# Optimization experiments

Hardware: AMD Instinct MI355X
Metric: run time of the kernel (lower is better)

The kernel has to match this reference:

```python
import jax, jax.numpy as jnp
from jax import lax
import numpy as np

NF = 64      # feature channels
G = 8        # deformable groups
K = 3        # kernel size
KK = K * K
NLEVEL = 3

PARAM_SHAPES = {
    "c0a_w": (64, 3, 3, 3), "c0a_b": (64,),
    "c0r_w1": (64, 64, 3, 3), "c0r_b1": (64,), "c0r_w2": (64, 64, 3, 3), "c0r_b2": (64,),
    "c0b_w": (64, 64, 3, 3), "c0b_b": (64,),
    "d_r1w1": (64, 64, 3, 3), "d_r1b1": (64,), "d_r1w2": (64, 64, 3, 3), "d_r1b2": (64,),
    "d_r2w1": (64, 64, 3, 3), "d_r2b1": (64,), "d_r2w2": (64, 64, 3, 3), "d_r2b2": (64,),
    "d_cw": (64, 64, 3, 3), "d_cb": (64,),
    "off_c1w": (64, 128, 3, 3), "off_c1b": (64,),
    "off_rw1": (64, 64, 3, 3), "off_rb1": (64,), "off_rw2": (64, 64, 3, 3), "off_rb2": (64,),
    "off_c2w": (64, 64, 3, 3), "off_c2b": (64,),
    "mrg_c1w": (64, 128, 3, 3), "mrg_c1b": (64,),
    "mrg_rw1": (64, 64, 3, 3), "mrg_rb1": (64,), "mrg_rw2": (64, 64, 3, 3), "mrg_rb2": (64,),
    "mrg_c2w": (64, 64, 3, 3), "mrg_c2b": (64,),
    "dcn_om_w": (216, 64, 3, 3), "dcn_om_b": (216,),
    "dcn_w": (64, 64, 3, 3), "dcn_b": (64,),
}


def setup_inputs() -> dict:
    key = jax.random.key(0)
    inp = {"images": jax.random.normal(key, (2, 3, 3, 160, 160), jnp.float32)}
    for i, (name, sh) in enumerate(PARAM_SHAPES.items()):
        if len(sh) == 1:
            inp[name] = jnp.zeros(sh, jnp.float32)
        else:
            inp[name] = jax.random.normal(jax.random.fold_in(key, i + 1), sh, jnp.float32) * 0.05
    return inp


def conv(x, w, b):
    y = lax.conv_general_dilated(x, w, (1, 1), 'SAME',
                                 dimension_numbers=('NCHW', 'OIHW', 'NCHW'))
    return y + b[None, :, None, None]


def lrelu(x):  # nn.LeakyReLU default slope 0.01
    return jnp.where(x >= 0, x, 0.01 * x)


def resblock(x, w1, b1, w2, b2):
    return x + conv(jax.nn.relu(conv(x, w1, b1)), w2, b2)


def maxpool3s2(x):  # MaxPool2d(3, 2, 1)
    return lax.reduce_window(x, -jnp.inf, lax.max, (1, 1, 3, 3), (1, 1, 2, 2),
                             ((0, 0), (0, 0), (1, 1), (1, 1)))


def offnet(x, c1w, c1b, rw1, rb1, rw2, rb2, c2w, c2b):
    # Conv-LReLU, then the SAME residual block applied twice (shared), Conv-LReLU
    x = lrelu(conv(x, c1w, c1b))
    x = resblock(x, rw1, rb1, rw2, rb2)
    x = resblock(x, rw1, rb1, rw2, rb2)
    return lrelu(conv(x, c2w, c2b))


def dcn(x, feat, om_w, om_b, w, b):
    # Modulated deformable conv v2 (extra_offset_mask=True): offsets/mask from feat.
    B, C, H, W = x.shape
    Cg = C // G
    om = conv(feat, om_w, om_b)                       # [B, 3*G*KK, H, W]
    o1, o2, m = jnp.split(om, 3, axis=1)
    dy = o1.reshape(B, G, KK, H, W)
    dx = o2.reshape(B, G, KK, H, W)
    mask = jax.nn.sigmoid(m).reshape(B, G, KK, H, W)
    ky, kx = jnp.meshgrid(jnp.arange(K, dtype=x.dtype) - 1,
                          jnp.arange(K, dtype=x.dtype) - 1, indexing='ij')
    py = dy + jnp.arange(H, dtype=x.dtype)[:, None] + ky.reshape(KK)[:, None, None]
    px = dx + jnp.arange(W, dtype=x.dtype) + kx.reshape(KK)[:, None, None]
    y0 = jnp.floor(py); x0 = jnp.floor(px)
    wy = py - y0; wx = px - x0
    y0i = y0.astype(jnp.int32); x0i = x0.astype(jnp.int32)
    xg = x.reshape(B, G, Cg, H * W)

    def gather(yi, xi, wt):
        valid = (yi >= 0) & (yi < H) & (xi >= 0) & (xi < W)
        idx = jnp.clip(yi, 0, H - 1) * W + jnp.clip(xi, 0, W - 1)      # [B,G,KK,H,W]
        g = jnp.take_along_axis(
            xg, jnp.broadcast_to(idx.reshape(B, G, 1, KK * H * W), (B, G, Cg, KK * H * W)),
            axis=3).reshape(B, G, Cg, KK, H, W)
        return g * (wt * valid)[:, :, None]

    val = (gather(y0i, x0i, (1 - wy) * (1 - wx))
           + gather(y0i, x0i + 1, (1 - wy) * wx)
           + gather(y0i + 1, x0i, wy * (1 - wx))
           + gather(y0i + 1, x0i + 1, wy * wx))
    val = val * mask[:, :, None]                      # [B,G,Cg,KK,H,W]
    wr = w.reshape(w.shape[0], G, Cg, KK)
    return jnp.einsum('bgckhw,ogck->bohw', val, wr) + b[None, :, None, None]


def reference(images, c0a_w, c0a_b, c0r_w1, c0r_b1, c0r_w2, c0r_b2, c0b_w, c0b_b,
              d_r1w1, d_r1b1, d_r1w2, d_r1b2, d_r2w1, d_r2b1, d_r2w2, d_r2b2, d_cw, d_cb,
              off_c1w, off_c1b, off_rw1, off_rb1, off_rw2, off_rb2, off_c2w, off_c2b,
              mrg_c1w, mrg_c1b, mrg_rw1, mrg_rb1, mrg_rw2, mrg_rb2, mrg_c2w, mrg_c2b,
              dcn_om_w, dcn_om_b, dcn_w, dcn_b):
    b, n, c, h, w = images.shape
    x = images.reshape(b * n, c, h, w)
    x = conv(x, c0a_w, c0a_b)
    x = resblock(x, c0r_w1, c0r_b1, c0r_w2, c0r_b2)
    feat = lrelu(conv(x, c0b_w, c0b_b))
    pyrs = [feat]
    for _ in range(NLEVEL - 1):  # downs share one parameter set ([module]*n)
        y = resblock(pyrs[-1], d_r1w1, d_r1b1, d_r1w2, d_r1b2)
        y = resblock(y, d_r2w1, d_r2b1, d_r2w2, d_r2b2)
        y = lrelu(maxpool3s2(conv(y, d_cw, d_cb)))
        pyrs.append(y)
    laps = [p.reshape(b, n, NF, p.shape[-2], p.shape[-1]) for p in pyrs]
    offp = (off_c1w, off_c1b, off_rw1, off_rb1, off_rw2, off_rb2, off_c2w, off_c2b)
    mrgp = (mrg_c1w, mrg_c1b, mrg_rw1, mrg_rb1, mrg_rw2, mrg_rb2, mrg_c2w, mrg_c2b)
    cv = n // 2
    for view in range(n):  # sequential in-place update (center view mutates mid-loop)
        po = offnet(jnp.concatenate([laps[-1][:, cv], laps[-1][:, view]], 1), *offp)
        laps[-1] = laps[-1].at[:, view].set(
            dcn(laps[-1][:, view], po, dcn_om_w, dcn_om_b, dcn_w, dcn_b))
        for level in range(NLEVEL - 2, -1, -1):
            cf = laps[level][:, cv]
            lf = laps[level][:, view]
            off = offnet(jnp.concatenate([cf, lf], 1), *offp)
            B_, C_, H_, W_ = po.shape
            po_up = jax.image.resize(po, (B_, C_, H_ * 2, W_ * 2), 'bilinear')
            off = offnet(jnp.concatenate([off, po_up * 2.0], 1), *mrgp)
            laps[level] = laps[level].at[:, view].set(
                dcn(lf, off, dcn_om_w, dcn_om_b, dcn_w, dcn_b))
            po = off
    return tuple(laps)
```

## Files before the change

### kernel.cpp

```cpp
#include <hip/hip_runtime.h>
#include <math.h>

using short8 = __attribute__((ext_vector_type(8))) short;
using f32x4  = __attribute__((ext_vector_type(4))) float;

struct Tab8 { long o[8]; };

__device__ __forceinline__ unsigned short f2bf(float f) {
    unsigned u = __builtin_bit_cast(unsigned, f);
    unsigned r = u + 0x7FFFu + ((u >> 16) & 1u);
    return (unsigned short)(r >> 16);
}
__device__ __forceinline__ float bf2f(unsigned short h) {
    unsigned u = ((unsigned)h) << 16;
    return __builtin_bit_cast(float, u);
}

struct WDesc { const float* w; int Ci, O, Opad; long off; };
struct WDescs { WDesc d[18]; };

__global__ __launch_bounds__(256) void prep_w_k(WDescs ds, unsigned short* wp)
{
    const WDesc d = ds.d[blockIdx.y];
    const int ncib = (d.Ci + 15) >> 4;
    const int n = ncib * d.Opad * 288;
    const int idx = blockIdx.x * 256 + threadIdx.x;
    if (idx >= n) return;
    const int within = idx % 288;
    const int o = (idx / 288) % d.Opad;
    const int cib = idx / (288 * d.Opad);
    const int t = within >> 5, q = within & 31;
    const int ci = (cib << 4) + (q & 15);
    float v = 0.0f;
    if (o < d.O && ci < d.Ci) v = d.w[((long)o * d.Ci + ci) * 9 + t];
    const unsigned short hi = f2bf(v);
    const unsigned short lo = f2bf(v - bf2f(hi));
    wp[d.off + idx] = (q < 16) ? hi : lo;
}

__global__ __launch_bounds__(256) void prep_dcnw_k(const float* __restrict__ w,
                                                   unsigned short* __restrict__ out)
{
    const int idx = blockIdx.x * 256 + threadIdx.x;
    if (idx >= 36 * 64 * 32) return;
    const int q = idx & 31, o = (idx >> 5) & 63, kb = idx >> 11;
    const float v = w[o * 576 + kb * 16 + (q & 15)];
    const unsigned short hi = f2bf(v);
    out[idx] = (q < 16) ? hi : f2bf(v - bf2f(hi));
}

__global__ __launch_bounds__(256, 2) void conv_mfma_k(
    const float* __restrict__ in1, Tab8 t1, int cin1,
    const float* __restrict__ in2, Tab8 t2, int cin2,
    const unsigned short* __restrict__ wp,
    const float* __restrict__ bias,
    const float* __restrict__ res, Tab8 trr, int hasres,
    float* __restrict__ out, Tab8 to,
    int O, int H, int W, int act)
{
    __shared__ unsigned short in_t[12960];
    __shared__ unsigned short w_t[18944];
    const int tid = threadIdx.x;
    const int b = blockIdx.z;
    const int Opad = gridDim.y << 6;
    const int cobase = blockIdx.y << 6;
    const int tilesX = (W + 15) >> 4;
    const int tx = blockIdx.x % tilesX, ty = blockIdx.x / tilesX;
    const int x0 = tx << 4, y0 = ty << 4;
    const int HW = H * W;
    const int cin_tot = cin1 + cin2;
    const int ncib = (cin_tot + 15) >> 4;
    const int wv = tid >> 6, lane = tid & 63;
    const int lxx = lane & 15, kb = lane >> 4;
    const long o1 = t1.o[b], o2 = t2.o[b];

    f32x4 acc[4][4];
    #pragma unroll
    for (int i = 0; i < 4; ++i)
        #pragma unroll
        for (int j = 0; j < 4; ++j)
            acc[i][j] = (f32x4){0.f, 0.f, 0.f, 0.f};

    for (int cib = 0; cib < ncib; ++cib) {
        __syncthreads();
        const unsigned short* slab = wp + ((long)cib * Opad + cobase) * 288;
        #pragma unroll
        for (int i = 0; i < 9; ++i) {
            const int c = tid + (i << 8);
            const int row = c / 36, col = c - row * 36;
            *(short8*)&w_t[row * 296 + (col << 3)] =
                *(const short8*)(slab + row * 288 + (col << 3));
        }
        if (tid < 144) {
            const int yy = tid >> 3, rp = tid & 7;
            const int g = (cib << 4) + (rp << 1);
            const float* s0 = nullptr;
            const float* s1 = nullptr;
            if (g < cin_tot)
                s0 = (g < cin1) ? in1 + o1 + (long)g * HW
                                : in2 + o2 + (long)(g - cin1) * HW;
            if (g + 1 < cin_tot)
                s1 = (g + 1 < cin1) ? in1 + o1 + (long)(g + 1) * HW
                                    : in2 + o2 + (long)(g + 1 - cin1) * HW;
            const int gy = y0 - 1 + yy;
            const bool yok = (gy >= 0) && (gy < H);
            #pragma unroll
            for (int xx = 0; xx < 18; ++xx) {
                const int gx = x0 - 1 + xx;
                const bool ok = yok && (gx >= 0) && (gx < W);
                const float v0 = (ok && s0) ? s0[gy * W + gx] : 0.0f;
                const float v1 = (ok && s1) ? s1[gy * W + gx] : 0.0f;
                const unsigned short h0 = f2bf(v0), h1 = f2bf(v1);
                const unsigned short l0 = f2bf(v0 - bf2f(h0));
                const unsigned short l1 = f2bf(v1 - bf2f(h1));
                unsigned short* base = &in_t[(yy * 18 + xx) * 40];
                *(unsigned*)(base + (rp << 1))      = (unsigned)h0 | ((unsigned)h1 << 16);
                *(unsigned*)(base + 16 + (rp << 1)) = (unsigned)l0 | ((unsigned)l1 << 16);
            }
        }
        __syncthreads();
        #pragma unroll
        for (int ky = 0; ky < 3; ++ky) {
            #pragma unroll
            for (int kx = 0; kx < 3; ++kx) {
                const int tap = ky * 3 + kx;
                short8 a[4], b1[4], b2[4];
                #pragma unroll
                for (int mt = 0; mt < 4; ++mt)
                    a[mt] = *(const short8*)&w_t[(mt * 16 + lxx) * 296 + tap * 32 + kb * 8];
                #pragma unroll
                for (int rr = 0; rr < 4; ++rr) {
                    const int pbase = ((wv * 4 + rr + ky) * 18 + lxx + kx) * 40;
                    b1[rr] = *(const short8*)&in_t[pbase + kb * 8];
                    b2[rr] = *(const short8*)&in_t[pbase + (kb ^ 2) * 8];
                }
                #pragma unroll
                for (int mt = 0; mt < 4; ++mt)
                    #pragma unroll
                    for (int rr = 0; rr < 4; ++rr) {
                        acc[mt][rr] = __builtin_amdgcn_mfma_f32_16x16x32_bf16(
                            a[mt], b1[rr], acc[mt][rr], 0, 0, 0);
                        acc[mt][rr] = __builtin_amdgcn_mfma_f32_16x16x32_bf16(
                            a[mt], b2[rr], acc[mt][rr], 0, 0, 0);
                    }
            }
        }
    }

    const int x = x0 + lxx;
    const bool xok = (x < W);
    const long ob = to.o[b], rb = trr.o[b];
    #pragma unroll
    for (int mt = 0; mt < 4; ++mt) {
        const int col0 = cobase + mt * 16 + kb * 4;
        float bvv[4];
        #pragma unroll
        for (int j = 0; j < 4; ++j)
            bvv[j] = (col0 + j < O) ? bias[col0 + j] : 0.0f;
        #pragma unroll
        for (int rr = 0; rr < 4; ++rr) {
            const int y = y0 + wv * 4 + rr;
            if (y >= H) continue;
            #pragma unroll
            for (int j = 0; j < 4; ++j) {
                const int coj = col0 + j;
                if (coj >= O || !xok) continue;
                float v = acc[mt][rr][j] + bvv[j];
                if (hasres) v += res[rb + (long)coj * HW + (long)y * W + x];
                if (act == 1) v = fmaxf(v, 0.0f);
                else if (act == 2) v = (v >= 0.0f) ? v : 0.01f * v;
                out[ob + (long)coj * HW + (long)y * W + x] = v;
            }
        }
    }
}

__global__ __launch_bounds__(256) void pool_lrelu_k(
    const float* __restrict__ in, float* __restrict__ out, int H, int W)
{
    const int Ho = H / 2, Wo = W / 2;
    const int n = blockIdx.y;
    const int i = blockIdx.x * 256 + threadIdx.x;
    if (i >= Ho * Wo) return;
    const int ho = i / Wo, wo = i % Wo;
    const float* p = in + (long)n * H * W;
    float m = -1e30f;
    #pragma unroll
    for (int dy = 0; dy < 3; ++dy) {
        const int y = 2 * ho - 1 + dy;
        if (y < 0 || y >= H) continue;
        #pragma unroll
        for (int dx = 0; dx < 3; ++dx) {
            const int x = 2 * wo - 1 + dx;
            if (x < 0 || x >= W) continue;
            m = fmaxf(m, p[y * W + x]);
        }
    }
    out[(long)n * Ho * Wo + i] = (m >= 0.0f) ? m : 0.01f * m;
}

__global__ __launch_bounds__(256) void resize2x_k(
    const float* __restrict__ in, float* __restrict__ out, int H, int W)
{
    const int Ho = 2 * H, Wo = 2 * W;
    const int n = blockIdx.y;
    const int i = blockIdx.x * 256 + threadIdx.x;
    if (i >= Ho * Wo) return;
    const int ho = i / Wo, wo = i % Wo;
    float cy = fminf(fmaxf(0.5f * (ho + 0.5f) - 0.5f, 0.0f), (float)(H - 1));
    float cx = fminf(fmaxf(0.5f * (wo + 0.5f) - 0.5f, 0.0f), (float)(W - 1));
    const int y0 = (int)cy, x0 = (int)cx;
    const int y1 = min(y0 + 1, H - 1), x1 = min(x0 + 1, W - 1);
    const float fy = cy - y0, fx = cx - x0;
    const float* p = in + (long)n * H * W;
    const float v = (1.0f - fy) * ((1.0f - fx) * p[y0 * W + x0] + fx * p[y0 * W + x1])
                  + fy * ((1.0f - fx) * p[y1 * W + x0] + fx * p[y1 * W + x1]);
    out[(long)n * Ho * Wo + i] = 2.0f * v;
}

__global__ __launch_bounds__(256) void copy_view_k(
    const float* __restrict__ src, float* __restrict__ dst, Tab8 td, int n)
{
    const int i = blockIdx.x * 256 + threadIdx.x;
    const int b = blockIdx.y;
    if (i < n) dst[td.o[b] + i] = src[(long)b * n + i];
}

__global__ __launch_bounds__(256, 2) void dcn_mfma_k(
    const float* __restrict__ xbase, Tab8 xoff,
    const float* __restrict__ om, long omstride,
    const unsigned short* __restrict__ wp,
    const float* __restrict__ bias,
    float* __restrict__ out, long ostride,
    int H, int W)
{
    __shared__ unsigned short valb[9][32][40];
    __shared__ unsigned short wblk[9][64][40];
    float* rw4 = (float*)&wblk[0][0][0];
    int* ridx = (int*)(rw4 + 576 * 4);
    int* rdd  = ridx + 576;

    const int tid = threadIdx.x;
    const int vb = blockIdx.y;
    const int HW = H * W;
    const int pos0 = blockIdx.x * 32;
    const float* xv = xbase + xoff.o[vb];
    const float* omv = om + (long)vb * omstride;
    const int lane = tid & 63, wv = tid >> 6;
    const int lxx = lane & 15, kq = lane >> 4;
    const int sp = tid >> 3, sc = tid & 7;

    f32x4 acc[2];
    acc[0] = (f32x4){0.f, 0.f, 0.f, 0.f};
    acc[1] = (f32x4){0.f, 0.f, 0.f, 0.f};

    for (int gp = 0; gp < 4; ++gp) {
        __syncthreads();
        for (int r = tid; r < 576; r += 256) {
            const int p = r & 31;
            const int gk = r >> 5;
            const int g2 = (gk >= 9) ? 1 : 0;
            const int kk = gk - g2 * 9;
            const int g = gp * 2 + g2;
            const int pos = pos0 + p;
            const int hh = pos / W, ww = pos % W;
            const int ch = g * 9 + kk;
            const float dy = omv[(long)ch * HW + pos];
            const float dx = omv[(long)(72 + ch) * HW + pos];
            const float mv = omv[(long)(144 + ch) * HW + pos];
            const float m = 1.0f / (1.0f + expf(-mv));
            float py = dy + (float)(hh + kk / 3 - 1);
            float px = dx + (float)(ww + kk % 3 - 1);
            py = fminf(fmaxf(py, -8.0f), (float)H + 8.0f);
            px = fminf(fmaxf(px, -8.0f), (float)W + 8.0f);
            const float yf = floorf(py), xf = floorf(px);
            const float wy = py - yf, wx = px - xf;
            const int y0 = (int)yf, x0 = (int)xf;
            const int y1 = y0 + 1, x1 = x0 + 1;
            const bool yv0 = (y0 >= 0) && (y0 < H), yv1 = (y1 >= 0) && (y1 < H);
            const bool xv0_ = (x0 >= 0) && (x0 < W), xv1_ = (x1 >= 0) && (x1 < W);
            const int yc0 = min(max(y0, 0), H - 1), yc1 = min(max(y1, 0), H - 1);
            const int xc0 = min(max(x0, 0), W - 1), xc1 = min(max(x1, 0), W - 1);
            rw4[r * 4 + 0] = (yv0 && xv0_) ? (1.f - wy) * (1.f - wx) * m : 0.f;
            rw4[r * 4 + 1] = (yv0 && xv1_) ? (1.f - wy) * wx * m : 0.f;
            rw4[r * 4 + 2] = (yv1 && xv0_) ? wy * (1.f - wx) * m : 0.f;
            rw4[r * 4 + 3] = (yv1 && xv1_) ? wy * wx * m : 0.f;
            ridx[r] = yc0 * W + xc0;
            rdd[r] = (xc1 - xc0) | (((yc1 - yc0) * W) << 8);
        }
        __syncthreads();
        #pragma unroll
        for (int g2 = 0; g2 < 2; ++g2) {
            const int g = gp * 2 + g2;
            const float* xc = xv + (long)(g * 8 + sc) * HW;
            const int kbase = g * 72 + sc * 9;
            #pragma unroll
            for (int kk = 0; kk < 9; ++kk) {
                const int r = (g2 * 9 + kk) * 32 + sp;
                const float4 w4 = *(const float4*)&rw4[r * 4];
                const int i00 = ridx[r];
                const int dd = rdd[r];
                const int dx01 = dd & 0xff, dyW = dd >> 8;
                const float v = w4.x * xc[i00] + w4.y * xc[i00 + dx01]
                              + w4.z * xc[i00 + dyW] + w4.w * xc[i00 + dyW + dx01];
                const int k = kbase + kk;
                const int q = k & 15;
                const int kb = (k >> 4) - gp * 9;
                const unsigned short hi = f2bf(v);
                valb[kb][sp][q] = hi;
                valb[kb][sp][q + 16] = f2bf(v - bf2f(hi));
            }
        }
        __syncthreads();
        {
            const unsigned short* src = wp + (long)gp * 9 * 64 * 32;
            #pragma unroll
            for (int i = 0; i < 9; ++i) {
                const int c = tid + (i << 8);
                const int kb = c >> 8, within = c & 255;
                const int o = within >> 2, part = within & 3;
                *(short8*)&wblk[kb][o][part * 8] =
                    *(const short8*)(src + ((kb * 64 + o) * 32 + part * 8));
            }
        }
        __syncthreads();
        #pragma unroll
        for (int kb = 0; kb < 9; ++kb) {
            const short8 a = *(const short8*)&wblk[kb][wv * 16 + lxx][kq * 8];
            #pragma unroll
            for (int pt = 0; pt < 2; ++pt) {
                const short8 b1 = *(const short8*)&valb[kb][pt * 16 + lxx][kq * 8];
                const short8 b2 = *(const short8*)&valb[kb][pt * 16 + lxx][(kq ^ 2) * 8];
                acc[pt] = __builtin_amdgcn_mfma_f32_16x16x32_bf16(a, b1, acc[pt], 0, 0, 0);
                acc[pt] = __builtin_amdgcn_mfma_f32_16x16x32_bf16(a, b2, acc[pt], 0, 0, 0);
            }
        }
    }
    float* ov = out + (long)vb * ostride;
    #pragma unroll
    for (int pt = 0; pt < 2; ++pt)
        #pragma unroll
        for (int j = 0; j < 4; ++j) {
            const int o = wv * 16 + kq * 4 + j;
            const int p = pt * 16 + lxx;
            ov[(long)o * HW + pos0 + p] = acc[pt][j] + bias[o];
        }
}

namespace {

struct MOff {
    const unsigned short *c1w; const float* c1b;
    const unsigned short *rw1; const float* rb1;
    const unsigned short *rw2; const float* rb2;
    const unsigned short *c2w; const float* c2b;
};

inline Tab8 tab(long stride) {
    Tab8 t;
    for (int i = 0; i < 8; ++i) t.o[i] = (long)i * stride;
    return t;
}

inline void conv_b(hipStream_t s,
                   const float* i1, Tab8 t1, int c1,
                   const float* i2, Tab8 t2, int c2,
                   const unsigned short* w, const float* bias,
                   const float* res, Tab8 trr, int hasres,
                   float* out, Tab8 to,
                   int O, int Opad, int H, int W, int B, int act)
{
    dim3 grid(((H + 15) / 16) * ((W + 15) / 16), Opad / 64, B);
    conv_mfma_k<<<grid, 256, 0, s>>>(i1, t1, c1, i2, t2, c2, w, bias,
                                     res, trr, hasres, out, to, O, H, W, act);
}

inline void offnetB(hipStream_t s, const MOff& p,
                    const float* cfb, Tab8 tcf, const float* lfb, Tab8 tlf,
                    float* t1, float* u, float* outp, int H, int W, int B)
{
    const long hw = (long)H * W;
    const Tab8 tz = tab(64 * hw);
    conv_b(s, cfb, tcf, 64, lfb, tlf, 64, p.c1w, p.c1b,
           nullptr, tz, 0, t1, tz, 64, 64, H, W, B, 2);
    for (int r = 0; r < 2; ++r) {
        conv_b(s, t1, tz, 64, nullptr, tz, 0, p.rw1, p.rb1,
               nullptr, tz, 0, u, tz, 64, 64, H, W, B, 1);
        conv_b(s, u, tz, 64, nullptr, tz, 0, p.rw2, p.rb2,
               t1, tz, 1, t1, tz, 64, 64, H, W, B, 0);
    }
    conv_b(s, t1, tz, 64, nullptr, tz, 0, p.c2w, p.c2b,
           nullptr, tz, 0, outp, tz, 64, 64, H, W, B, 2);
}

inline void dcnB(hipStream_t s, const float* lapbase, Tab8 tlf,
                 const float* feat,
                 const unsigned short* Wom, const float* omb,
                 const unsigned short* Wdcn, const float* dcnb,
                 float* om, float* tmp, int H, int W, int VB)
{
    const long hw = (long)H * W;
    const long cap = 8L * 64 * 25600;
    int cmax = (int)(cap / (216 * hw));
    if (cmax > VB) cmax = VB;
    if (cmax < 1) cmax = 1;
    for (int c0 = 0; c0 < VB; c0 += cmax) {
        const int nc = (VB - c0 < cmax) ? (VB - c0) : cmax;
        Tab8 tfeat = tab(0), tx = tab(0), tdst = tab(0);
        for (int i = 0; i < nc; ++i) {
            tfeat.o[i] = (long)(c0 + i) * 64 * hw;
            tx.o[i]    = tlf.o[c0 + i];
            tdst.o[i]  = tlf.o[c0 + i];
        }
        conv_b(s, feat, tfeat, 64, nullptr, tfeat, 0, Wom, omb,
               nullptr, tfeat, 0, om, tab(216 * hw), 216, 256, H, W, nc, 0);
        dim3 gd((int)(hw / 32), nc);
        dcn_mfma_k<<<gd, 256, 0, s>>>(lapbase, tx, om, 216 * hw, Wdcn, dcnb,
                                      tmp, 64 * hw, H, W);
        dim3 gc((int)((64 * hw + 255) / 256), nc);
        copy_view_k<<<gc, 256, 0, s>>>(tmp, (float*)lapbase, tdst, (int)(64 * hw));
    }
}

}

extern "C" void kernel_launch(void* const* d_in, const int* in_sizes, int n_in,
                              void* d_out, int out_size, void* d_ws, size_t ws_size,
                              hipStream_t stream)
{
    (void)in_sizes; (void)n_in; (void)out_size; (void)ws_size;
    const float* P[39];
    for (int k = 0; k < 39; ++k) P[k] = (const float*)d_in[k];
    const float* images = P[0];

    const int HW0 = 160 * 160, HW1 = 80 * 80, HW2 = 40 * 40;
    float* L0 = (float*)d_out;
    float* L1 = L0 + (long)6 * 64 * HW0;
    float* L2 = L1 + (long)6 * 64 * HW1;

    const long SZ = (long)64 * HW0;
    float* ws = (float*)d_ws;
    float* OFF_A = ws;
    float* OFF_B = ws + 4 * SZ;
    float* POUP  = ws + 8 * SZ;
    float* T1    = ws + 12 * SZ;
    float* U     = POUP;
    float* OM    = ws + 8 * SZ;
    float* A     = ws;
    float* Bb    = ws + 6 * SZ;
    unsigned short* WP = (unsigned short*)(ws + 16 * SZ);

    const int widx[18] = {1,3,5,7,9,11,13,15,17,19,21,23,25,27,29,31,33,35};
    const int wci[18]  = {3,64,64,64,64,64,64,64,64,128,64,64,64,128,64,64,64,64};
    const int wo_[18]  = {64,64,64,64,64,64,64,64,64,64,64,64,64,64,64,64,64,216};
    WDescs ds;
    long off = 0;
    long woff[18];
    for (int i = 0; i < 18; ++i) {
        const int opad = (wo_[i] + 63) / 64 * 64;
        const int ncib = (wci[i] + 15) / 16;
        ds.d[i].w = P[widx[i]]; ds.d[i].Ci = wci[i]; ds.d[i].O = wo_[i];
        ds.d[i].Opad = opad; ds.d[i].off = off;
        woff[i] = off;
        off += (long)ncib * opad * 288;
    }
    unsigned short* WPD = WP + off;
    prep_w_k<<<dim3(1152, 18), 256, 0, stream>>>(ds, WP);
    prep_dcnw_k<<<dim3(288), 256, 0, stream>>>(P[37], WPD);

    const unsigned short* Wc0a  = WP + woff[0];
    const unsigned short* Wc0r1 = WP + woff[1];
    const unsigned short* Wc0r2 = WP + woff[2];
    const unsigned short* Wc0b  = WP + woff[3];
    const unsigned short* Wd11  = WP + woff[4];
    const unsigned short* Wd12  = WP + woff[5];
    const unsigned short* Wd21  = WP + woff[6];
    const unsigned short* Wd22  = WP + woff[7];
    const unsigned short* Wdc   = WP + woff[8];
    MOff offp = {WP + woff[9],  P[20], WP + woff[10], P[22],
                 WP + woff[11], P[24], WP + woff[12], P[26]};
    MOff mrgp = {WP + woff[13], P[28], WP + woff[14], P[30],
                 WP + woff[15], P[32], WP + woff[16], P[34]};
    const unsigned short* Wom = WP + woff[17];
    const float* dcn_om_b = P[36];
    const float* dcn_b = P[38];

    const Tab8 ti = tab((long)3 * HW0);
    const Tab8 t60 = tab((long)64 * HW0);
    const Tab8 t61 = tab((long)64 * HW1);
    conv_b(stream, images, ti, 3, nullptr, t60, 0, Wc0a, P[2],
           nullptr, t60, 0, A, t60, 64, 64, 160, 160, 6, 0);
    conv_b(stream, A, t60, 64, nullptr, t60, 0, Wc0r1, P[4],
           nullptr, t60, 0, Bb, t60, 64, 64, 160, 160, 6, 1);
    conv_b(stream, Bb, t60, 64, nullptr, t60, 0, Wc0r2, P[6],
           A, t60, 1, A, t60, 64, 64, 160, 160, 6, 0);
    conv_b(stream, A, t60, 64, nullptr, t60, 0, Wc0b, P[8],
           nullptr, t60, 0, L0, t60, 64, 64, 160, 160, 6, 2);

    conv_b(stream, L0, t60, 64, nullptr, t60, 0, Wd11, P[10],
           nullptr, t60, 0, Bb, t60, 64, 64, 160, 160, 6, 1);
    conv_b(stream, Bb, t60, 64, nullptr, t60, 0, Wd12, P[12],
           L0, t60, 1, A, t60, 64, 64, 160, 160, 6, 0);
    conv_b(stream, A, t60, 64, nullptr, t60, 0, Wd21, P[14],
           nullptr, t60, 0, Bb, t60, 64, 64, 160, 160, 6, 1);
    conv_b(stream, Bb, t60, 64, nullptr, t60, 0, Wd22, P[16],
           A, t60, 1, A, t60, 64, 64, 160, 160, 6, 0);
    conv_b(stream, A, t60, 64, nullptr, t60, 0, Wdc, P[18],
           nullptr, t60, 0, Bb, t60, 64, 64, 160, 160, 6, 0);
    {
        dim3 gp((HW1 + 255) / 256, 6 * 64);
        pool_lrelu_k<<<gp, 256, 0, stream>>>(Bb, L1, 160, 160);
    }
    conv_b(stream, L1, t61, 64, nullptr, t61, 0, Wd11, P[10],
           nullptr, t61, 0, Bb, t61, 64, 64, 80, 80, 6, 1);
    conv_b(stream, Bb, t61, 64, nullptr, t61, 0, Wd12, P[12],
           L1, t61, 1, A, t61, 64, 64, 80, 80, 6, 0);
    conv_b(stream, A, t61, 64, nullptr, t61, 0, Wd21, P[14],
           nullptr, t61, 0, Bb, t61, 64, 64, 80, 80, 6, 1);
    conv_b(stream, Bb, t61, 64, nullptr, t61, 0, Wd22, P[16],
           A, t61, 1, A, t61, 64, 64, 80, 80, 6, 0);
    conv_b(stream, A, t61, 64, nullptr, t61, 0, Wdc, P[18],
           nullptr, t61, 0, Bb, t61, 64, 64, 80, 80, 6, 0);
    {
        dim3 gp((HW2 + 255) / 256, 6 * 64);
        pool_lrelu_k<<<gp, 256, 0, stream>>>(Bb, L2, 80, 80);
    }

    const int cv = 1;
    for (int pass = 0; pass < 2; ++pass) {
        const int vs01[2] = {0, 1};
        const int vs2[1] = {2};
        const int* vlist = pass ? vs2 : vs01;
        const int nv = pass ? 1 : 2;
        const int VB = nv * 2;

        Tab8 tcf2 = tab(0), tlf2 = tab(0), tcf1 = tab(0), tlf1 = tab(0),
             tcf0 = tab(0), tlf0 = tab(0);
        for (int i = 0; i < VB; ++i) {
            const int v = vlist[i >> 1], b = i & 1;
            tlf2.o[i] = ((long)b * 3 + v)  * 64 * HW2;
            tcf2.o[i] = ((long)b * 3 + cv) * 64 * HW2;
            tlf1.o[i] = ((long)b * 3 + v)  * 64 * HW1;
            tcf1.o[i] = ((long)b * 3 + cv) * 64 * HW1;
            tlf0.o[i] = ((long)b * 3 + v)  * 64 * HW0;
            tcf0.o[i] = ((long)b * 3 + cv) * 64 * HW0;
        }
        offnetB(stream, offp, L2, tcf2, L2, tlf2, T1, U, OFF_A, 40, 40, VB);
        dcnB(stream, L2, tlf2, OFF_A, Wom, dcn_om_b, WPD, dcn_b,
             OM, OFF_B, 40, 40, VB);
        offnetB(stream, offp, L1, tcf1, L1, tlf1, T1, U, OFF_B, 80, 80, VB);
        {
            dim3 gr((HW1 + 255) / 256, VB * 64);
            resize2x_k<<<gr, 256, 0, stream>>>(OFF_A, POUP, 40, 40);
        }
        offnetB(stream, mrgp, OFF_B, tab((long)64 * HW1), POUP, tab((long)64 * HW1),
                T1, U, OFF_A, 80, 80, VB);
        dcnB(stream, L1, tlf1, OFF_A, Wom, dcn_om_b, WPD, dcn_b,
             OM, OFF_B, 80, 80, VB);
        offnetB(stream, offp, L0, tcf0, L0, tlf0, T1, U, OFF_B, 160, 160, VB);
        {
            dim3 gr((HW0 + 255) / 256, VB * 64);
            resize2x_k<<<gr, 256, 0, stream>>>(OFF_A, POUP, 80, 80);
        }
        offnetB(stream, mrgp, OFF_B, tab((long)64 * HW0), POUP, tab((long)64 * HW0),
                T1, U, OFF_A, 160, 160, VB);
        dcnB(stream, L0, tlf0, OFF_A, Wom, dcn_om_b, WPD, dcn_b,
             OM, OFF_B, 160, 160, VB);
    }
}
```

Before: 6.755 ms.

## Transpose DCN input to NHWC, write output in place, restructure staging loads

The deformable conv input view is first transposed to NHWC in a workspace buffer. Each bilinear tap can then load 8 contiguous group channels with float4 reads instead of scattered per-channel gathers. The DCN kernel now writes straight into the pyramid view, which removes the separate copy kernel, and it reads weights from global memory instead of staging them through shared memory. The conv input-tile staging is also spread over all 256 threads rather than 144. The cost is an extra transpose pass, workspace for the transposed copy, and uncached global weight reads inside the MFMA loop.

```diff
diff --git a/kernel.cpp b/kernel.cpp
--- a/kernel.cpp
+++ b/kernel.cpp
@@ -91,25 +91,26 @@
             *(short8*)&w_t[row * 296 + (col << 3)] =
                 *(const short8*)(slab + row * 288 + (col << 3));
         }
-        if (tid < 144) {
-            const int yy = tid >> 3, rp = tid & 7;
-            const int g = (cib << 4) + (rp << 1);
-            const float* s0 = nullptr;
-            const float* s1 = nullptr;
-            if (g < cin_tot)
-                s0 = (g < cin1) ? in1 + o1 + (long)g * HW
-                                : in2 + o2 + (long)(g - cin1) * HW;
-            if (g + 1 < cin_tot)
-                s1 = (g + 1 < cin1) ? in1 + o1 + (long)(g + 1) * HW
-                                    : in2 + o2 + (long)(g + 1 - cin1) * HW;
-            const int gy = y0 - 1 + yy;
-            const bool yok = (gy >= 0) && (gy < H);
-            #pragma unroll
-            for (int xx = 0; xx < 18; ++xx) {
+        for (int it = 0; it < 11; ++it) {
+            const int idx = it * 256 + tid;
+            if (idx < 2592) {
+                const int xx = idx % 18;
+                const int yy = (idx / 18) % 18;
+                const int rp = idx / 324;
+                const int g = (cib << 4) + (rp << 1);
+                const int gy = y0 - 1 + yy;
                 const int gx = x0 - 1 + xx;
-                const bool ok = yok && (gx >= 0) && (gx < W);
-                const float v0 = (ok && s0) ? s0[gy * W + gx] : 0.0f;
-                const float v1 = (ok && s1) ? s1[gy * W + gx] : 0.0f;
+                const bool ok = (gy >= 0) && (gy < H) && (gx >= 0) && (gx < W);
+                float v0 = 0.f, v1 = 0.f;
+                if (ok) {
+                    const long pix = (long)gy * W + gx;
+                    if (g < cin_tot)
+                        v0 = (g < cin1) ? in1[o1 + (long)g * HW + pix]
+                                        : in2[o2 + (long)(g - cin1) * HW + pix];
+                    if (g + 1 < cin_tot)
+                        v1 = (g + 1 < cin1) ? in1[o1 + (long)(g + 1) * HW + pix]
+                                            : in2[o2 + (long)(g + 1 - cin1) * HW + pix];
+                }
                 const unsigned short h0 = f2bf(v0), h1 = f2bf(v1);
                 const unsigned short l0 = f2bf(v0 - bf2f(h0));
                 const unsigned short l1 = f2bf(v1 - bf2f(h1));
@@ -218,44 +219,56 @@
     out[(long)n * Ho * Wo + i] = 2.0f * v;
 }
 
-__global__ __launch_bounds__(256) void copy_view_k(
-    const float* __restrict__ src, float* __restrict__ dst, Tab8 td, int n)
-{
-    const int i = blockIdx.x * 256 + threadIdx.x;
-    const int b = blockIdx.y;
-    if (i < n) dst[td.o[b] + i] = src[(long)b * n + i];
+__global__ __launch_bounds__(256) void nhwc_k(
+    const float* __restrict__ src, Tab8 ts, float* __restrict__ dst,
+    long dstride, int HW)
+{
+    __shared__ float t[64][65];
+    const int tid = threadIdx.x;
+    const int vb = blockIdx.y;
+    const int pos0 = blockIdx.x * 64;
+    const float* s = src + ts.o[vb];
+    float* d = dst + (long)vb * dstride;
+    const int l = tid & 63, q = tid >> 6;
+    #pragma unroll
+    for (int i = 0; i < 16; ++i) {
+        const int c = q * 16 + i;
+        t[c][l] = s[(long)c * HW + pos0 + l];
+    }
+    __syncthreads();
+    #pragma unroll
+    for (int i = 0; i < 16; ++i) {
+        const int p = q * 16 + i;
+        d[(long)(pos0 + p) * 64 + l] = t[l][p];
+    }
 }
 
 __global__ __launch_bounds__(256, 2) void dcn_mfma_k(
-    const float* __restrict__ xbase, Tab8 xoff,
+    const float* __restrict__ xT, long xtstride,
     const float* __restrict__ om, long omstride,
     const unsigned short* __restrict__ wp,
     const float* __restrict__ bias,
-    float* __restrict__ out, long ostride,
+    float* __restrict__ outb, Tab8 toff,
     int H, int W)
 {
     __shared__ unsigned short valb[9][32][40];
-    __shared__ unsigned short wblk[9][64][40];
-    float* rw4 = (float*)&wblk[0][0][0];
-    int* ridx = (int*)(rw4 + 576 * 4);
-    int* rdd  = ridx + 576;
+    __shared__ float rw0[576], rw1[576], rw2[576], rw3[576];
+    __shared__ int ridx[576], rdd[576];
 
     const int tid = threadIdx.x;
     const int vb = blockIdx.y;
     const int HW = H * W;
     const int pos0 = blockIdx.x * 32;
-    const float* xv = xbase + xoff.o[vb];
+    const float* xv = xT + (long)vb * xtstride;
     const float* omv = om + (long)vb * omstride;
     const int lane = tid & 63, wv = tid >> 6;
     const int lxx = lane & 15, kq = lane >> 4;
-    const int sp = tid >> 3, sc = tid & 7;
 
     f32x4 acc[2];
     acc[0] = (f32x4){0.f, 0.f, 0.f, 0.f};
     acc[1] = (f32x4){0.f, 0.f, 0.f, 0.f};
 
     for (int gp = 0; gp < 4; ++gp) {
-        __syncthreads();
         for (int r = tid; r < 576; r += 256) {
             const int p = r & 31;
             const int gk = r >> 5;
@@ -281,62 +294,68 @@
             const bool xv0_ = (x0 >= 0) && (x0 < W), xv1_ = (x1 >= 0) && (x1 < W);
             const int yc0 = min(max(y0, 0), H - 1), yc1 = min(max(y1, 0), H - 1);
             const int xc0 = min(max(x0, 0), W - 1), xc1 = min(max(x1, 0), W - 1);
-            rw4[r * 4 + 0] = (yv0 && xv0_) ? (1.f - wy) * (1.f - wx) * m : 0.f;
-            rw4[r * 4 + 1] = (yv0 && xv1_) ? (1.f - wy) * wx * m : 0.f;
-            rw4[r * 4 + 2] = (yv1 && xv0_) ? wy * (1.f - wx) * m : 0.f;
-            rw4[r * 4 + 3] = (yv1 && xv1_) ? wy * wx * m : 0.f;
+            rw0[r] = (yv0 && xv0_) ? (1.f - wy) * (1.f - wx) * m : 0.f;
+            rw1[r] = (yv0 && xv1_) ? (1.f - wy) * wx * m : 0.f;
+            rw2[r] = (yv1 && xv0_) ? wy * (1.f - wx) * m : 0.f;
+            rw3[r] = (yv1 && xv1_) ? wy * wx * m : 0.f;
             ridx[r] = yc0 * W + xc0;
             rdd[r] = (xc1 - xc0) | (((yc1 - yc0) * W) << 8);
         }
         __syncthreads();
-        #pragma unroll
-        for (int g2 = 0; g2 < 2; ++g2) {
+        for (int r = tid; r < 576; r += 256) {
+            const int p = r & 31;
+            const int gk = r >> 5;
+            const int g2 = (gk >= 9) ? 1 : 0;
+            const int kk = gk - g2 * 9;
             const int g = gp * 2 + g2;
-            const float* xc = xv + (long)(g * 8 + sc) * HW;
-            const int kbase = g * 72 + sc * 9;
-            #pragma unroll
-            for (int kk = 0; kk < 9; ++kk) {
-                const int r = (g2 * 9 + kk) * 32 + sp;
-                const float4 w4 = *(const float4*)&rw4[r * 4];
-                const int i00 = ridx[r];
-                const int dd = rdd[r];
-                const int dx01 = dd & 0xff, dyW = dd >> 8;
-                const float v = w4.x * xc[i00] + w4.y * xc[i00 + dx01]
-                              + w4.z * xc[i00 + dyW] + w4.w * xc[i00 + dyW + dx01];
-                const int k = kbase + kk;
-                const int q = k & 15;
-                const int kb = (k >> 4) - gp * 9;
-                const unsigned short hi = f2bf(v);
-                valb[kb][sp][q] = hi;
-                valb[kb][sp][q + 16] = f2bf(v - bf2f(hi));
-            }
+            const float w0 = rw0[r], w1 = rw1[r], w2 = rw2[r], w3 = rw3[r];
+            const int dd = rdd[r];
+            const long b00 = ((long)ridx[r] << 6) + (g << 3);
+            const long d01 = (long)(dd & 0xff) << 6;
+            const long d10 = (long)(dd >> 8) << 6;
+            const float4 aA = *(const float4*)(xv + b00);
+            const float4 aB = *(const float4*)(xv + b00 + 4);
+            const float4 bA = *(const float4*)(xv + b00 + d01);
+            const float4 bB = *(const float4*)(xv + b00 + d01 + 4);
+            const float4 cA = *(const float4*)(xv + b00 + d10);
+            const float4 cB = *(const float4*)(xv + b00 + d10 + 4);
+            const float4 dA = *(const float4*)(xv + b00 + d10 + d01);
+            const float4 dB = *(const float4*)(xv + b00 + d10 + d01 + 4);
+            const int kb0 = g * 72 + kk;
+#define DO_CH(VAL, C) { \
+            const float v_ = (VAL); \
+            const int k_ = kb0 + 9 * (C); \
+            const int kbl_ = (k_ >> 4) - gp * 9; \
+            const int q_ = k_ & 15; \
+            const unsigned short hi_ = f2bf(v_); \
+            valb[kbl_][p][q_] = hi_; \
+            valb[kbl_][p][q_ + 16] = f2bf(v_ - bf2f(hi_)); }
+            DO_CH(w0 * aA.x + w1 * bA.x + w2 * cA.x + w3 * dA.x, 0)
+            DO_CH(w0 * aA.y + w1 * bA.y + w2 * cA.y + w3 * dA.y, 1)
+            DO_CH(w0 * aA.z + w1 * bA.z + w2 * cA.z + w3 * dA.z, 2)
+            DO_CH(w0 * aA.w + w1 * bA.w + w2 * cA.w + w3 * dA.w, 3)
+            DO_CH(w0 * aB.x + w1 * bB.x + w2 * cB.x + w3 * dB.x, 4)
+            DO_CH(w0 * aB.y + w1 * bB.y + w2 * cB.y + w3 * dB.y, 5)
+            DO_CH(w0 * aB.z + w1 * bB.z + w2 * cB.z + w3 * dB.z, 6)
+            DO_CH(w0 * aB.w + w1 * bB.w + w2 * cB.w + w3 * dB.w, 7)
+#undef DO_CH
         }
         __syncthreads();
-        {
-            const unsigned short* src = wp + (long)gp * 9 * 64 * 32;
-            #pragma unroll
-            for (int i = 0; i < 9; ++i) {
-                const int c = tid + (i << 8);
-                const int kb = c >> 8, within = c & 255;
-                const int o = within >> 2, part = within & 3;
-                *(short8*)&wblk[kb][o][part * 8] =
-                    *(const short8*)(src + ((kb * 64 + o) * 32 + part * 8));
-            }
-        }
-        __syncthreads();
         #pragma unroll
         for (int kb = 0; kb < 9; ++kb) {
-            const short8 a = *(const short8*)&wblk[kb][wv * 16 + lxx][kq * 8];
+            const short8 a = *(const short8*)(
+                wp + ((long)(gp * 9 + kb) * 64 + wv * 16 + lxx) * 32 + kq * 8);
             #pragma unroll
             for (int pt = 0; pt < 2; ++pt) {
-                const short8 b1 = *(const short8*)&valb[kb][pt * 16 + lxx][kq * 8];
-                const short8 b2 = *(const short8*)&valb[kb][pt * 16 + lxx][(kq ^ 2) * 8];
-                acc[pt] = __builtin_amdgcn_mfma_f32_16x16x32_bf16(a, b1, acc[pt], 0, 0, 0);
-                acc[pt] = __builtin_amdgcn_mfma_f32_16x16x32_bf16(a, b2, acc[pt], 0, 0, 0);
+                const short8 v1 = *(const short8*)&valb[kb][pt * 16 + lxx][kq * 8];
+                const short8 v2 = *(const short8*)&valb[kb][pt * 16 + lxx][(kq ^ 2) * 8];
+                acc[pt] = __builtin_amdgcn_mfma_f32_16x16x32_bf16(a, v1, acc[pt], 0, 0, 0);
+                acc[pt] = __builtin_amdgcn_mfma_f32_16x16x32_bf16(a, v2, acc[pt], 0, 0, 0);
             }
         }
-    }
-    float* ov = out + (long)vb * ostride;
+        __syncthreads();
+    }
+    float* ov = outb + toff.o[vb];
     #pragma unroll
     for (int pt = 0; pt < 2; ++pt)
         #pragma unroll
@@ -393,32 +412,33 @@
            nullptr, tz, 0, outp, tz, 64, 64, H, W, B, 2);
 }
 
-inline void dcnB(hipStream_t s, const float* lapbase, Tab8 tlf,
+inline void dcnB(hipStream_t s, float* lapbase, Tab8 tlf,
                  const float* feat,
                  const unsigned short* Wom, const float* omb,
                  const unsigned short* Wdcn, const float* dcnb,
-                 float* om, float* tmp, int H, int W, int VB)
+                 float* om, float* xt, int H, int W, int VB)
 {
     const long hw = (long)H * W;
-    const long cap = 8L * 64 * 25600;
-    int cmax = (int)(cap / (216 * hw));
+    const long SZf = 64L * 25600;
+    int cmax = (int)((8L * SZf) / (216 * hw));
+    const int cx = (int)((4L * SZf) / (64 * hw));
+    if (cx < cmax) cmax = cx;
     if (cmax > VB) cmax = VB;
     if (cmax < 1) cmax = 1;
     for (int c0 = 0; c0 < VB; c0 += cmax) {
         const int nc = (VB - c0 < cmax) ? (VB - c0) : cmax;
-        Tab8 tfeat = tab(0), tx = tab(0), tdst = tab(0);
+        Tab8 tfeat = tab(0), tx = tab(0);
         for (int i = 0; i < nc; ++i) {
             tfeat.o[i] = (long)(c0 + i) * 64 * hw;
             tx.o[i]    = tlf.o[c0 + i];
-            tdst.o[i]  = tlf.o[c0 + i];
-        }
+        }
+        dim3 gt((int)(hw / 64), nc);
+        nhwc_k<<<gt, 256, 0, s>>>(lapbase, tx, xt, 64 * hw, (int)hw);
         conv_b(s, feat, tfeat, 64, nullptr, tfeat, 0, Wom, omb,
                nullptr, tfeat, 0, om, tab(216 * hw), 216, 256, H, W, nc, 0);
         dim3 gd((int)(hw / 32), nc);
-        dcn_mfma_k<<<gd, 256, 0, s>>>(lapbase, tx, om, 216 * hw, Wdcn, dcnb,
-                                      tmp, 64 * hw, H, W);
-        dim3 gc((int)((64 * hw + 255) / 256), nc);
-        copy_view_k<<<gc, 256, 0, s>>>(tmp, (float*)lapbase, tdst, (int)(64 * hw));
+        dcn_mfma_k<<<gd, 256, 0, s>>>(xt, 64 * hw, om, 216 * hw, Wdcn, dcnb,
+                                      lapbase, tx, H, W);
     }
 }
 
```

Result: slower. 10.32 ms (+52.8%).
